# Kernel optimization log

Measured on AMD Instinct MI355X. Metric: run time of the kernel, lower is better.

Reference implementation:

```python
import jax, jax.numpy as jnp
import numpy as np

B, H, W, C = 16, 56, 56, 384
NH, WS = 12, 7
N = WS * WS
NW = (H // WS) * (W // WS)
SHIFTS = (0, WS // 2)
HD = C // NH
SCALE = HD ** -0.5


def _rel_idx():
    ch, cw = np.meshgrid(np.arange(WS), np.arange(WS), indexing='ij')
    cf = np.stack([ch.ravel(), cw.ravel()])            # (2, N)
    rc = cf[:, :, None] - cf[:, None, :]               # (2, N, N)
    rc = rc.transpose(1, 2, 0).copy()
    rc[:, :, 0] += WS - 1
    rc[:, :, 1] += WS - 1
    rc[:, :, 0] *= 2 * WS - 1
    return rc.sum(-1).astype(np.int32)                 # (N, N)


def _attn_mask(shift):
    img = np.zeros((H, W))
    sl = (slice(0, -WS), slice(-WS, -shift), slice(-shift, None))
    cnt = 0
    for hs in sl:
        for ws_ in sl:
            img[hs, ws_] = cnt
            cnt += 1
    mw = img.reshape(H // WS, WS, W // WS, WS).transpose(0, 2, 1, 3).reshape(-1, N)
    d = mw[:, None, :] - mw[:, :, None]
    return np.where(d != 0, -100.0, 0.0).astype(np.float32)  # (NW, N, N)


def setup_inputs() -> dict:
    key = jax.random.key(0)
    ks = jax.random.split(key, 8)
    p = lambda k, shape: (jax.random.normal(k, shape, jnp.float32) * 0.02)
    return dict(
        x=jax.random.normal(ks[0], (B, H, W, C), jnp.float32),
        attn_mask=jnp.asarray(_attn_mask(SHIFTS[1])),
        rel_idx=jnp.asarray(_rel_idx()),
        norm1_g=jnp.ones((2, C), jnp.float32),
        norm1_b=jnp.zeros((2, C), jnp.float32),
        qkv_w=p(ks[1], (2, 3 * C, C)),
        qkv_b=jnp.zeros((2, 3 * C), jnp.float32),
        rpb=p(ks[2], (2, (2 * WS - 1) ** 2, NH)),
        proj_w=p(ks[3], (2, C, C)),
        proj_b=jnp.zeros((2, C), jnp.float32),
        norm2_g=jnp.ones((2, C), jnp.float32),
        norm2_b=jnp.zeros((2, C), jnp.float32),
        fc1_w=p(ks[4], (2, 4 * C, C)),
        fc1_b=jnp.zeros((2, 4 * C), jnp.float32),
        fc2_w=p(ks[5], (2, C, 4 * C)),
        fc2_b=jnp.zeros((2, C), jnp.float32),
    )


def _ln(x, g, b):
    m = x.mean(-1, keepdims=True)
    v = x.var(-1, keepdims=True)
    return (x - m) * jax.lax.rsqrt(v + 1e-5) * g + b


def _partition(x):
    # (B,H,W,C) -> (B*nW, N, C)
    x = x.reshape(B, H // WS, WS, W // WS, WS, C)
    return x.transpose(0, 1, 3, 2, 4, 5).reshape(-1, N, C)


def _reverse(w):
    # (B*nW, N, C) -> (B,H,W,C)
    w = w.reshape(B, H // WS, W // WS, WS, WS, C)
    return w.transpose(0, 1, 3, 2, 4, 5).reshape(B, H, W, C)


def reference(x, attn_mask, rel_idx, norm1_g, norm1_b, qkv_w, qkv_b, rpb,
              proj_w, proj_b, norm2_g, norm2_b, fc1_w, fc1_b, fc2_w, fc2_b):
    for i, shift in enumerate(SHIFTS):
        shortcut = x.reshape(B, H * W, C)
        xn = _ln(shortcut, norm1_g[i], norm1_b[i]).reshape(B, H, W, C)
        if shift > 0:
            xn = jnp.roll(xn, (-shift, -shift), (1, 2))
        xw = _partition(xn)                               # (B_, N, C)
        qkv = xw @ qkv_w[i].T + qkv_b[i]                  # (B_, N, 3C)
        qkv = qkv.reshape(-1, N, 3, NH, HD).transpose(2, 0, 3, 1, 4)
        q, k, v = qkv[0], qkv[1], qkv[2]                  # (B_, NH, N, HD)
        attn = jnp.einsum('bhnd,bhmd->bhnm', q * SCALE, k)
        bias = rpb[i][rel_idx.reshape(-1)].reshape(N, N, NH).transpose(2, 0, 1)
        attn = attn + bias[None]
        if shift > 0:
            attn = attn.reshape(B, NW, NH, N, N) + attn_mask[None, :, None]
            attn = attn.reshape(-1, NH, N, N)
        attn = jax.nn.softmax(attn, axis=-1)
        out = jnp.einsum('bhnm,bhmd->bhnd', attn, v)
        out = out.transpose(0, 2, 1, 3).reshape(-1, N, C)
        out = out @ proj_w[i].T + proj_b[i]
        sx = _reverse(out)
        if shift > 0:
            sx = jnp.roll(sx, (shift, shift), (1, 2))
        x = shortcut + sx.reshape(B, H * W, C)
        h = jax.nn.gelu(_ln(x, norm2_g[i], norm2_b[i]) @ fc1_w[i].T + fc1_b[i],
                        approximate=False)
        x = x + (h @ fc2_w[i].T + fc2_b[i])
        x = x.reshape(B, H, W, C)
    return x
```

## Files before the change

### kernel.cpp

```cpp
#include <hip/hip_runtime.h>
#include <hip/hip_fp8.h>
#include <math.h>

typedef unsigned char  u8;
typedef unsigned short u16;
typedef unsigned int   u32;
typedef long long      i64;
typedef __attribute__((ext_vector_type(4))) float f32x4;
typedef __attribute__((ext_vector_type(8))) short bf16x8;

#define M_TOK 50176
#define CDIM  384

__device__ __forceinline__ u16 f2b(float f){
  union { float f; u32 u; } v; v.f = f;
  u32 r = v.u + 0x7fffu + ((v.u >> 16) & 1u);
  return (u16)(r >> 16);
}
__device__ __forceinline__ u32 pack2(float a, float b){
  return (u32)f2b(a) | ((u32)f2b(b) << 16);
}
__device__ __forceinline__ u8 f2q(float v){
  __hip_fp8_e4m3 t(v);
  return *reinterpret_cast<u8*>(&t);
}

__device__ __forceinline__ void gload_lds16(const void* g, void* l){
  __builtin_amdgcn_global_load_lds((const __attribute__((address_space(1))) u32*)g,
                                   (__attribute__((address_space(3))) u32*)l, 16, 0, 0);
}

__global__ void cvtw(const float* __restrict__ in, u16* __restrict__ out, int n4){
  int i = blockIdx.x * 256 + threadIdx.x;
  if (i < n4){
    float4 v = ((const float4*)in)[i];
    uint2 o; o.x = pack2(v.x, v.y); o.y = pack2(v.z, v.w);
    ((uint2*)out)[i] = o;
  }
}
__global__ void cvtw8(const float* __restrict__ in, u8* __restrict__ out, int n4){
  int i = blockIdx.x * 256 + threadIdx.x;
  if (i < n4){
    float4 v = ((const float4*)in)[i];
    u32 o = (u32)f2q(v.x) | ((u32)f2q(v.y) << 8) |
            ((u32)f2q(v.z) << 16) | ((u32)f2q(v.w) << 24);
    ((u32*)out)[i] = o;
  }
}

template<int F8>
__global__ __launch_bounds__(256) void ln_kernel(
    const float* __restrict__ x, const float* __restrict__ g,
    const float* __restrict__ b, void* __restrict__ out, int ntok)
{
  int wave = threadIdx.x >> 6, lane = threadIdx.x & 63;
  for (long t = blockIdx.x * 4 + wave; t < ntok; t += (long)gridDim.x * 4){
    const float* xr = x + t * CDIM;
    float v[6]; float s = 0.f, ss = 0.f;
    #pragma unroll
    for (int j = 0; j < 6; ++j){ v[j] = xr[j*64 + lane]; s += v[j]; ss += v[j]*v[j]; }
    #pragma unroll
    for (int o = 32; o >= 1; o >>= 1){ s += __shfl_xor(s, o); ss += __shfl_xor(ss, o); }
    float mean = s * (1.f/384.f);
    float var  = ss * (1.f/384.f) - mean*mean;
    float rs   = rsqrtf(var + 1e-5f);
    #pragma unroll
    for (int j = 0; j < 6; ++j){
      int c = j*64 + lane;
      float val = (v[j] - mean) * rs * g[c] + b[c];
      if (F8) ((u8*)out)[t*CDIM + c] = f2q(val);
      else    ((u16*)out)[t*CDIM + c] = f2b(val);
    }
  }
}

template<int EPI>
__global__ __launch_bounds__(256, 4) void gemm_bt(
    const u16* __restrict__ A, const u16* __restrict__ Wt,
    const float* __restrict__ bias, const float* __restrict__ resid,
    void* __restrict__ outp, int M, int N, int K)
{
  __shared__ __align__(16) u16 smem[16384];
  const int tid  = threadIdx.x;
  const int wave = tid >> 6, lane = tid & 63;
  const int nbn  = N >> 7;
  const int nwg = gridDim.x;
  const int q8 = nwg >> 3, r8 = nwg & 7, xcd = blockIdx.x & 7, o8 = blockIdx.x >> 3;
  const int sid = (xcd < r8 ? xcd*(q8+1) : r8*(q8+1) + (xcd-r8)*q8) + o8;
  const int bm = sid / nbn, bn = sid % nbn;
  const int wr = wave >> 1, wc = wave & 1;
  const int l15 = lane & 15, l4 = lane >> 4;
  const int srow = tid >> 2, sch = tid & 3;

  f32x4 acc[4][4] = {};

  auto STAGE = [&](int buf, int kt){
    u16* lAp = smem + buf*4096;
    u16* lBp = smem + 8192 + buf*4096;
    #pragma unroll
    for (int it = 0; it < 2; ++it){
      int row = it*64 + srow;
      int chs = sch ^ ((srow >> 1) & 3);
      const u16* ga = A  + (size_t)(bm*128 + row) * K + kt + chs*8;
      const u16* gb = Wt + (size_t)(bn*128 + row) * K + kt + chs*8;
      gload_lds16(ga, &lAp[(it*256 + wave*64) * 8]);
      gload_lds16(gb, &lBp[(it*256 + wave*64) * 8]);
    }
  };

  const int NK = K >> 5;
  STAGE(0, 0);

  int cur = 0;
  for (int ki = 0; ki < NK; ++ki){
    if (ki + 1 < NK){
      STAGE(cur ^ 1, (ki + 1) * 32);
      asm volatile("s_waitcnt vmcnt(4)" ::: "memory");
    } else {
      asm volatile("s_waitcnt vmcnt(0)" ::: "memory");
    }
    __builtin_amdgcn_s_barrier();
    const u16* lAp = smem + cur*4096;
    const u16* lBp = smem + 8192 + cur*4096;
    bf16x8 af[4], bfr[4];
    const int rc = (l4 ^ ((l15 >> 1) & 3)) * 8;
    #pragma unroll
    for (int mi = 0; mi < 4; ++mi)
      af[mi] = *(const bf16x8*)&lAp[(wr*64 + mi*16 + l15)*32 + rc];
    #pragma unroll
    for (int ni = 0; ni < 4; ++ni)
      bfr[ni] = *(const bf16x8*)&lBp[(wc*64 + ni*16 + l15)*32 + rc];
    #pragma unroll
    for (int mi = 0; mi < 4; ++mi)
      #pragma unroll
      for (int ni = 0; ni < 4; ++ni)
        acc[mi][ni] = __builtin_amdgcn_mfma_f32_16x16x32_bf16(af[mi], bfr[ni], acc[mi][ni], 0, 0, 0);
    __builtin_amdgcn_s_barrier();
    cur ^= 1;
  }

  if (EPI == 2){
    #pragma unroll
    for (int ni = 0; ni < 4; ++ni){
      int col = bn*128 + wc*64 + ni*16 + l15;
      float bb = bias[col];
      #pragma unroll
      for (int mi = 0; mi < 4; ++mi){
        int row0 = bm*128 + wr*64 + mi*16 + l4*4;
        #pragma unroll
        for (int r = 0; r < 4; ++r){
          long off = (long)(row0 + r) * N + col;
          ((float*)outp)[off] = resid[off] + acc[mi][ni][r] + bb;
        }
      }
    }
  } else {
    #pragma unroll
    for (int ni = 0; ni < 4; ++ni){
      int colL = wc*64 + ni*16 + l15;
      float bb = bias[bn*128 + colL];
      int colS = colL ^ (l4*16);
      #pragma unroll
      for (int mi = 0; mi < 4; ++mi){
        int rowL = wr*64 + mi*16 + l4*4;
        #pragma unroll
        for (int r = 0; r < 4; ++r){
          float v = acc[mi][ni][r] + bb;
          smem[(rowL + r)*128 + colS] = f2b(v);
        }
      }
    }
    __syncthreads();
    const u32* eb = (const u32*)smem;
    u32* og = (u32*)outp;
    const int nW = N >> 1;
    #pragma unroll
    for (int it = 0; it < 32; ++it){
      int row = wave*32 + it;
      u32 w = eb[row*64 + (lane ^ (((row >> 2) & 3) * 8))];
      __builtin_nontemporal_store(w, &og[(size_t)(bm*128 + row) * nW + bn*64 + lane]);
    }
  }
}

template<int EPI>
__global__ __launch_bounds__(256, 4) void gemm_f8(
    const u8* __restrict__ A, const u8* __restrict__ Wt,
    const float* __restrict__ bias, const float* __restrict__ resid,
    void* __restrict__ outp, int M, int N, int K)
{
  __shared__ __align__(16) u8 smem[16384];
  const int tid  = threadIdx.x;
  const int wave = tid >> 6, lane = tid & 63;
  const int nbn  = N >> 7;
  const int nwg = gridDim.x;
  const int q8 = nwg >> 3, r8 = nwg & 7, xcd = blockIdx.x & 7, o8 = blockIdx.x >> 3;
  const int sid = (xcd < r8 ? xcd*(q8+1) : r8*(q8+1) + (xcd-r8)*q8) + o8;
  const int bm = sid / nbn, bn = sid % nbn;
  const int wr = wave >> 1, wc = wave & 1;
  const int l15 = lane & 15, l4 = lane >> 4;
  const int srow = tid >> 1, sch = tid & 1;

  f32x4 acc[4][4] = {};

  auto STAGE = [&](int buf, int kt){
    const u8* ga = A  + (size_t)(bm*128 + srow) * K + kt + sch*16;
    const u8* gb = Wt + (size_t)(bn*128 + srow) * K + kt + sch*16;
    gload_lds16(ga, &smem[buf*8192 + tid*16]);
    gload_lds16(gb, &smem[buf*8192 + 4096 + tid*16]);
  };

  const int NK = K >> 5;
  STAGE(0, 0);

  int cur = 0;
  for (int ki = 0; ki < NK; ++ki){
    if (ki + 1 < NK){
      STAGE(cur ^ 1, (ki + 1) * 32);
      asm volatile("s_waitcnt vmcnt(2)" ::: "memory");
    } else {
      asm volatile("s_waitcnt vmcnt(0)" ::: "memory");
    }
    __builtin_amdgcn_s_barrier();
    const u8* lAp = smem + cur*8192;
    const u8* lBp = smem + cur*8192 + 4096;
    i64 af[4], bf[4];
    #pragma unroll
    for (int mi = 0; mi < 4; ++mi)
      af[mi] = *(const i64*)&lAp[(wr*64 + mi*16 + l15)*32 + l4*8];
    #pragma unroll
    for (int ni = 0; ni < 4; ++ni)
      bf[ni] = *(const i64*)&lBp[(wc*64 + ni*16 + l15)*32 + l4*8];
    #pragma unroll
    for (int mi = 0; mi < 4; ++mi)
      #pragma unroll
      for (int ni = 0; ni < 4; ++ni)
        acc[mi][ni] = __builtin_amdgcn_mfma_f32_16x16x32_fp8_fp8(af[mi], bf[ni], acc[mi][ni], 0, 0, 0);
    __builtin_amdgcn_s_barrier();
    cur ^= 1;
  }

  if (EPI == 2){
    #pragma unroll
    for (int ni = 0; ni < 4; ++ni){
      int col = bn*128 + wc*64 + ni*16 + l15;
      float bb = bias[col];
      #pragma unroll
      for (int mi = 0; mi < 4; ++mi){
        int row0 = bm*128 + wr*64 + mi*16 + l4*4;
        #pragma unroll
        for (int r = 0; r < 4; ++r){
          long off = (long)(row0 + r) * N + col;
          ((float*)outp)[off] = resid[off] + acc[mi][ni][r] + bb;
        }
      }
    }
  } else {
    u8* og = (u8*)outp;
    #pragma unroll
    for (int ni = 0; ni < 4; ++ni){
      int col = bn*128 + wc*64 + ni*16 + l15;
      float bb = bias[col];
      #pragma unroll
      for (int mi = 0; mi < 4; ++mi){
        int row0 = bm*128 + wr*64 + mi*16 + l4*4;
        #pragma unroll
        for (int r = 0; r < 4; ++r){
          float v = acc[mi][ni][r] + bb;
          v = 0.5f * v * (1.f + erff(v * 0.70710678118654752f));
          og[(size_t)(row0 + r) * N + col] = f2q(v);
        }
      }
    }
  }
}

__global__ void build_btbl(const float* __restrict__ rpb, const int* __restrict__ ridx,
                           float* __restrict__ btbl){
  int q = blockIdx.x & 63, h = blockIdx.x >> 6;
  int l = threadIdx.x;
  float v = -1e9f;
  if (q < 49){
    int key = (l & 3) * 16 + (l >> 2);
    if (key < 49) v = rpb[ridx[q*49 + key] * 12 + h];
  }
  btbl[(h*64 + q)*64 + l] = v;
}

template<int SHIFT>
__global__ __launch_bounds__(64) void attn_mfma(
    const u16* __restrict__ qkv, const float* __restrict__ btbl,
    u16* __restrict__ attn_out)
{
  __shared__ __align__(16) u16 p_lds[64*72];
  __shared__ __align__(16) u16 vt_lds[32*72];
  __shared__ int tok_lds[64];
  __shared__ int rid_lds[64];

  const int bid = blockIdx.x;
  const int h   = bid % 12;
  const int win = bid / 12;
  const int b   = win >> 6, wl = win & 63;
  const int wy  = wl >> 3,  wx = wl & 7;
  const int lane = threadIdx.x;
  const int l15 = lane & 15, l4 = lane >> 4;

  auto tokof = [&](int n)->int{
    int r = (n * 9363) >> 16;
    int c = n - r * 7;
    int hh = wy*7 + r + SHIFT; if (hh >= 56) hh -= 56;
    int ww = wx*7 + c + SHIFT; if (ww >= 56) ww -= 56;
    return b*3136 + hh*56 + ww;
  };

  {
    const int n  = lane;
    const int nc = n < 49 ? n : 48;
    const int t  = tokof(nc);
    tok_lds[n] = t;
    if (SHIFT){
      int r = (nc * 9363) >> 16, c = nc - r*7;
      int gh = wy*7 + r, gw = wx*7 + c;
      int rh = gh <= 48 ? 0 : (gh <= 52 ? 1 : 2);
      int rw = gw <= 48 ? 0 : (gw <= 52 ? 1 : 2);
      rid_lds[n] = rh*3 + rw;
    }
    const uint4* vp = (const uint4*)(qkv + (size_t)t*1152 + 768 + h*32);
    u32 w[16];
    #pragma unroll
    for (int j4 = 0; j4 < 4; ++j4){
      uint4 u = vp[j4];
      w[j4*4+0]=u.x; w[j4*4+1]=u.y; w[j4*4+2]=u.z; w[j4*4+3]=u.w;
    }
    if (n >= 49){
      #pragma unroll
      for (int j = 0; j < 16; ++j) w[j] = 0;
    }
    #pragma unroll
    for (int j = 0; j < 16; ++j){
      vt_lds[(2*j  )*72 + n] = (u16)(w[j] & 0xffffu);
      vt_lds[(2*j+1)*72 + n] = (u16)(w[j] >> 16);
    }
  }

  bf16x8 qa[4], kb[4];
  #pragma unroll
  for (int mi = 0; mi < 4; ++mi){
    int row = mi*16 + l15; int t = tokof(row < 49 ? row : 48);
    qa[mi] = *(const bf16x8*)(qkv + (size_t)t*1152 + h*32 + l4*8);
  }
  #pragma unroll
  for (int ni = 0; ni < 4; ++ni){
    int row = ni*16 + l15; int t = tokof(row < 49 ? row : 48);
    kb[ni] = *(const bf16x8*)(qkv + (size_t)t*1152 + 384 + h*32 + l4*8);
  }
  f32x4 s[4][4] = {};
  #pragma unroll
  for (int mi = 0; mi < 4; ++mi)
    #pragma unroll
    for (int ni = 0; ni < 4; ++ni)
      s[mi][ni] = __builtin_amdgcn_mfma_f32_16x16x32_bf16(qa[mi], kb[ni], s[mi][ni], 0, 0, 0);

  __syncthreads();

  int rid_k[4];
  if (SHIFT){
    #pragma unroll
    for (int ni = 0; ni < 4; ++ni) rid_k[ni] = rid_lds[ni*16 + l15];
  }

  const float* bt = btbl + h*4096;
  float den[4][4];
  #pragma unroll
  for (int mi = 0; mi < 4; ++mi){
    #pragma unroll
    for (int r = 0; r < 4; ++r){
      int q = mi*16 + l4*4 + r;
      f32x4 bq = *(const f32x4*)(bt + q*64 + l15*4);
      int ridq = 0;
      if (SHIFT) ridq = rid_lds[q];
      #pragma unroll
      for (int ni = 0; ni < 4; ++ni){
        float v = s[mi][ni][r] * 0.17677669529663687f + bq[ni];
        if (SHIFT) v += (ridq == rid_k[ni]) ? 0.f : -100.f;
        s[mi][ni][r] = v;
      }
      float m0 = fmaxf(fmaxf(s[mi][0][r], s[mi][1][r]), fmaxf(s[mi][2][r], s[mi][3][r]));
      #pragma unroll
      for (int o = 1; o <= 8; o <<= 1) m0 = fmaxf(m0, __shfl_xor(m0, o));
      float d0 = 0.f;
      #pragma unroll
      for (int ni = 0; ni < 4; ++ni){
        float e = __expf(s[mi][ni][r] - m0);
        s[mi][ni][r] = e; d0 += e;
      }
      #pragma unroll
      for (int o = 1; o <= 8; o <<= 1) d0 += __shfl_xor(d0, o);
      den[mi][r] = d0;
    }
  }

  #pragma unroll
  for (int mi = 0; mi < 4; ++mi)
    #pragma unroll
    for (int r = 0; r < 4; ++r){
      int q = mi*16 + l4*4 + r;
      #pragma unroll
      for (int ni = 0; ni < 4; ++ni)
        p_lds[q*72 + ni*16 + l15] = f2b(s[mi][ni][r]);
    }

  __syncthreads();

  f32x4 o2[4][2] = {};
  #pragma unroll
  for (int ks = 0; ks < 2; ++ks){
    bf16x8 vb[2];
    #pragma unroll
    for (int ni = 0; ni < 2; ++ni)
      vb[ni] = *(const bf16x8*)&vt_lds[(ni*16 + l15)*72 + ks*32 + l4*8];
    #pragma unroll
    for (int mi = 0; mi < 4; ++mi){
      bf16x8 pa = *(const bf16x8*)&p_lds[(mi*16 + l15)*72 + ks*32 + l4*8];
      #pragma unroll
      for (int ni = 0; ni < 2; ++ni)
        o2[mi][ni] = __builtin_amdgcn_mfma_f32_16x16x32_bf16(pa, vb[ni], o2[mi][ni], 0, 0, 0);
    }
  }

  #pragma unroll
  for (int mi = 0; mi < 4; ++mi){
    #pragma unroll
    for (int r = 0; r < 4; ++r){
      int q = mi*16 + l4*4 + r;
      if (q < 49){
        float inv = 1.f / den[mi][r];
        long t = tok_lds[q];
        #pragma unroll
        for (int ni = 0; ni < 2; ++ni){
          int d = ni*16 + l15;
          attn_out[t*384 + h*32 + d] = f2b(o2[mi][ni][r] * inv);
        }
      }
    }
  }
}

extern "C" void kernel_launch(void* const* d_in, const int* in_sizes, int n_in,
                              void* d_out, int out_size, void* d_ws, size_t ws_size,
                              hipStream_t stream)
{
  const float* x_in   = (const float*)d_in[0];
  const int*   relidx = (const int*)d_in[2];
  const float* n1g    = (const float*)d_in[3];
  const float* n1b    = (const float*)d_in[4];
  const float* qkvw   = (const float*)d_in[5];
  const float* qkvb   = (const float*)d_in[6];
  const float* rpb    = (const float*)d_in[7];
  const float* pw     = (const float*)d_in[8];
  const float* pb     = (const float*)d_in[9];
  const float* n2g    = (const float*)d_in[10];
  const float* n2b    = (const float*)d_in[11];
  const float* f1w    = (const float*)d_in[12];
  const float* f1b    = (const float*)d_in[13];
  const float* f2w    = (const float*)d_in[14];
  const float* f2bb   = (const float*)d_in[15];
  float* xout = (float*)d_out;

  char* ws = (char*)d_ws;
  u16* wqkv   = (u16*)ws; ws += (size_t)2*1152*384*2;
  u16* wproj  = (u16*)ws; ws += (size_t)2*384*384*2;
  u8*  wfc1q  = (u8*)ws;  ws += (size_t)2*1536*384;
  u8*  wfc2q  = (u8*)ws;  ws += (size_t)2*384*1536;
  u16* bufA   = (u16*)ws; ws += (size_t)M_TOK*1536*2;
  u16* bufB   = (u16*)ws; ws += (size_t)M_TOK*384*2;
  u8*  bufD   = (u8*)ws;  ws += (size_t)M_TOK*384;
  float* btbl = (float*)(bufA + (size_t)M_TOK*1152);
  u8* h8 = (u8*)bufA;

  {
    int n;
    n = 2*1152*384;  cvtw <<<dim3((n/4+255)/256), dim3(256), 0, stream>>>(qkvw, wqkv,  n/4);
    n = 2*384*384;   cvtw <<<dim3((n/4+255)/256), dim3(256), 0, stream>>>(pw,   wproj, n/4);
    n = 2*1536*384;  cvtw8<<<dim3((n/4+255)/256), dim3(256), 0, stream>>>(f1w,  wfc1q, n/4);
    n = 2*384*1536;  cvtw8<<<dim3((n/4+255)/256), dim3(256), 0, stream>>>(f2w,  wfc2q, n/4);
  }

  for (int i = 0; i < 2; ++i){
    const float* xi = (i == 0) ? x_in : xout;
    ln_kernel<0><<<dim3(2048), dim3(256), 0, stream>>>(xi, n1g + i*384, n1b + i*384, bufB, M_TOK);
    gemm_bt<0><<<dim3(3528), dim3(256), 0, stream>>>(
        bufB, wqkv + (size_t)i*1152*384, qkvb + i*1152, nullptr, bufA, M_TOK, 1152, 384);
    build_btbl<<<dim3(768), dim3(64), 0, stream>>>(rpb + (size_t)i*169*12, relidx, btbl);
    if (i == 0)
      attn_mfma<0><<<dim3(12288), dim3(64), 0, stream>>>(bufA, btbl, bufB);
    else
      attn_mfma<3><<<dim3(12288), dim3(64), 0, stream>>>(bufA, btbl, bufB);
    gemm_bt<2><<<dim3(1176), dim3(256), 0, stream>>>(
        bufB, wproj + (size_t)i*384*384, pb + i*384, xi, xout, M_TOK, 384, 384);
    ln_kernel<1><<<dim3(2048), dim3(256), 0, stream>>>(xout, n2g + i*384, n2b + i*384, bufD, M_TOK);
    gemm_f8<1><<<dim3(4704), dim3(256), 0, stream>>>(
        bufD, wfc1q + (size_t)i*1536*384, f1b + i*1536, nullptr, h8, M_TOK, 1536, 384);
    gemm_f8<2><<<dim3(1176), dim3(256), 0, stream>>>(
        h8, wfc2q + (size_t)i*384*1536, f2bb + i*384, xout, xout, M_TOK, 384, 1536);
  }
  (void)in_sizes; (void)n_in; (void)out_size; (void)ws_size;
}
```

Baseline: 957.0 us.

## Swizzle FP8 GEMM LDS tiles and stage GELU output through LDS

Adds an XOR swizzle to the 16-byte chunk placement in the FP8 GEMM's shared-memory staging, with matching precomputed read offsets, to cut LDS bank conflicts on fragment loads. The GELU epilogue now writes FP8 bytes into a padded LDS tile and then emits coalesced 32-bit nontemporal stores, replacing scattered single-byte global stores. Shared memory grows slightly, which could affect occupancy, and the epilogue adds a block-wide barrier.

```diff
diff --git a/kernel.cpp b/kernel.cpp
--- a/kernel.cpp
+++ b/kernel.cpp
@@ -189,7 +189,7 @@
     const float* __restrict__ bias, const float* __restrict__ resid,
     void* __restrict__ outp, int M, int N, int K)
 {
-  __shared__ __align__(16) u8 smem[16384];
+  __shared__ __align__(16) u8 smem[17408];
   const int tid  = threadIdx.x;
   const int wave = tid >> 6, lane = tid & 63;
   const int nbn  = N >> 7;
@@ -199,19 +199,34 @@
   const int bm = sid / nbn, bn = sid % nbn;
   const int wr = wave >> 1, wc = wave & 1;
   const int l15 = lane & 15, l4 = lane >> 4;
-  const int srow = tid >> 1, sch = tid & 1;
 
   f32x4 acc[4][4] = {};
 
+  const int gsl = tid ^ ((tid >> 3) & 7);
+  const int grow = gsl >> 1, gc16 = gsl & 1;
+
   auto STAGE = [&](int buf, int kt){
-    const u8* ga = A  + (size_t)(bm*128 + srow) * K + kt + sch*16;
-    const u8* gb = Wt + (size_t)(bn*128 + srow) * K + kt + sch*16;
+    const u8* ga = A  + (size_t)(bm*128 + grow) * K + kt + gc16*16;
+    const u8* gb = Wt + (size_t)(bn*128 + grow) * K + kt + gc16*16;
     gload_lds16(ga, &smem[buf*8192 + tid*16]);
     gload_lds16(gb, &smem[buf*8192 + 4096 + tid*16]);
   };
 
   const int NK = K >> 5;
   STAGE(0, 0);
+
+  const int c16 = l4 >> 1, half8 = (l4 & 1) * 8;
+  int spA[4], spB[4];
+  #pragma unroll
+  for (int mi = 0; mi < 4; ++mi){
+    int s = (wr*64 + mi*16 + l15)*2 + c16;
+    spA[mi] = (s ^ ((s >> 3) & 7)) * 16 + half8;
+  }
+  #pragma unroll
+  for (int ni = 0; ni < 4; ++ni){
+    int s = (wc*64 + ni*16 + l15)*2 + c16;
+    spB[ni] = (s ^ ((s >> 3) & 7)) * 16 + half8;
+  }
 
   int cur = 0;
   for (int ki = 0; ki < NK; ++ki){
@@ -227,10 +242,10 @@
     i64 af[4], bf[4];
     #pragma unroll
     for (int mi = 0; mi < 4; ++mi)
-      af[mi] = *(const i64*)&lAp[(wr*64 + mi*16 + l15)*32 + l4*8];
+      af[mi] = *(const i64*)&lAp[spA[mi]];
     #pragma unroll
     for (int ni = 0; ni < 4; ++ni)
-      bf[ni] = *(const i64*)&lBp[(wc*64 + ni*16 + l15)*32 + l4*8];
+      bf[ni] = *(const i64*)&lBp[spB[ni]];
     #pragma unroll
     for (int mi = 0; mi < 4; ++mi)
       #pragma unroll
@@ -256,21 +271,30 @@
       }
     }
   } else {
-    u8* og = (u8*)outp;
     #pragma unroll
     for (int ni = 0; ni < 4; ++ni){
-      int col = bn*128 + wc*64 + ni*16 + l15;
-      float bb = bias[col];
+      int col = wc*64 + ni*16 + l15;
+      float bb = bias[bn*128 + col];
       #pragma unroll
       for (int mi = 0; mi < 4; ++mi){
-        int row0 = bm*128 + wr*64 + mi*16 + l4*4;
+        int row0 = wr*64 + mi*16 + l4*4;
         #pragma unroll
         for (int r = 0; r < 4; ++r){
           float v = acc[mi][ni][r] + bb;
           v = 0.5f * v * (1.f + erff(v * 0.70710678118654752f));
-          og[(size_t)(row0 + r) * N + col] = f2q(v);
+          smem[(row0 + r)*132 + col] = f2q(v);
         }
       }
+    }
+    __syncthreads();
+    u32* og = (u32*)outp;
+    const int nW = N >> 2;
+    const int colu = tid & 31, rw = tid >> 5;
+    #pragma unroll
+    for (int it = 0; it < 16; ++it){
+      int row = it*8 + rw;
+      u32 w = *(const u32*)&smem[row*132 + colu*4];
+      __builtin_nontemporal_store(w, &og[(size_t)(bm*128 + row) * nW + bn*32 + colu]);
     }
   }
 }
```

Result: faster. 929.1 us (-2.9%).
